# Kernel optimization log

Measured on AMD Instinct MI355X. Metric: run time of the kernel, lower is better.

The kernel has to match this reference:

```python
import jax, jax.numpy as jnp
import numpy as np

D_IN = 2048
H1 = D_IN // 4      # 512
H2 = D_IN // 16     # 128
N_EXP = 8
N_CLS = 10
BATCH = 16384


def setup_inputs() -> dict:
    key = jax.random.key(0)
    ks = jax.random.split(key, 16)
    s = lambda k, shape, fan_in: jax.random.normal(k, shape, jnp.float32) / np.sqrt(fan_in)
    return {
        "fs": jax.random.normal(ks[0], (BATCH, D_IN // 2), jnp.float32),
        "fp": jax.random.normal(ks[1], (BATCH, D_IN // 2), jnp.float32),
        # gate MLP params (output = num_source, softmax)
        "gW1": s(ks[2], (D_IN, H1), D_IN), "gb1": jnp.zeros((H1,), jnp.float32),
        "gW2": s(ks[3], (H1, H2), H1),     "gb2": jnp.zeros((H2,), jnp.float32),
        "gW3": s(ks[4], (H2, N_EXP), H2), "gb3": jnp.zeros((N_EXP,), jnp.float32),
        # stacked expert MLP params (output = num classes, log_softmax)
        "eW1": s(ks[5], (N_EXP, D_IN, H1), D_IN), "eb1": jnp.zeros((N_EXP, H1), jnp.float32),
        "eW2": s(ks[6], (N_EXP, H1, H2), H1),     "eb2": jnp.zeros((N_EXP, H2), jnp.float32),
        "eW3": s(ks[7], (N_EXP, H2, N_CLS), H2),  "eb3": jnp.zeros((N_EXP, N_CLS), jnp.float32),
    }


def reference(fs, fp, gW1, gb1, gW2, gb2, gW3, gb3, eW1, eb1, eW2, eb2, eW3, eb3):
    features = jnp.concatenate([fs, fp], axis=-1)            # [B, D_IN]

    # Gate MLP on detached features (detach is a no-op for fwd), softmax output
    g = jax.nn.relu(features @ gW1 + gb1)
    g = jax.nn.relu(g @ gW2 + gb2)
    gate_outs = jax.nn.softmax(g @ gW3 + gb3, axis=-1)       # [B, E]

    # All experts as batched GEMMs over stacked weights, log_softmax output
    h = jax.nn.relu(jnp.einsum('bd,edh->beh', features, eW1) + eb1[None])   # [B, E, H1]
    h = jax.nn.relu(jnp.einsum('beh,ehk->bek', h, eW2) + eb2[None])         # [B, E, H2]
    logits = jnp.einsum('bek,eko->beo', h, eW3) + eb3[None]                 # [B, E, C]
    expert_outs = jax.nn.log_softmax(logits, axis=-1)                       # [B, E, C]

    # Gate-weighted sum over experts
    output = jnp.einsum('be,bec->bc', gate_outs, expert_outs)               # [B, C]
    return output, gate_outs
```

## Files before the change

kernel.cpp:

```cpp
#include <hip/hip_runtime.h>
#include <hip/hip_bf16.h>

#define B_SZ   16384
#define DIN    2048
#define H1_SZ  512
#define H2_SZ  128
#define N_EXP  8
#define N_CLS  10
#define N1     4608
#define N2     1152

typedef __attribute__((ext_vector_type(8))) __bf16 bf16x8;
typedef __attribute__((ext_vector_type(4))) float  floatx4;
typedef __attribute__((ext_vector_type(4))) short  short4v;
typedef __attribute__((ext_vector_type(8))) short  short8v;

__device__ __forceinline__ float bf2f(short s) {
  unsigned int u = ((unsigned int)(unsigned short)s) << 16;
  float f; __builtin_memcpy(&f, &u, 4); return f;
}

__global__ __launch_bounds__(256) void prep_kernel(
    const float* __restrict__ fs, const float* __restrict__ fp,
    const float* __restrict__ eW1, const float* __restrict__ gW1,
    const float* __restrict__ eW2, const float* __restrict__ gW2,
    __hip_bfloat16* __restrict__ X,
    __hip_bfloat16* __restrict__ W1T,
    __hip_bfloat16* __restrict__ W2T) {
  __shared__ float tbuf[32][33];
  const int b   = blockIdx.x;
  const int tid = threadIdx.x;

  if (b < 2048) {
    const int nf4 = B_SZ * (DIN / 4);
    const float4* fs4 = (const float4*)fs;
    const float4* fp4 = (const float4*)fp;
    for (int i = b * 256 + tid; i < nf4; i += 2048 * 256) {
      int c = i & 511;
      int row = i >> 9;
      float4 v = (c < 256) ? fs4[(size_t)row * 256 + c]
                           : fp4[(size_t)row * 256 + (c - 256)];
      union { short4v v4; __hip_bfloat16 h[4]; } u;
      u.h[0] = __float2bfloat16(v.x);
      u.h[1] = __float2bfloat16(v.y);
      u.h[2] = __float2bfloat16(v.z);
      u.h[3] = __float2bfloat16(v.w);
      *(short4v*)(X + (size_t)i * 4) = u.v4;
    }
  } else {
    const float* esrc; const float* gsrc; __hip_bfloat16* out;
    int K, H, bx, by;
    if (b < 2048 + 9216) {
      int t = b - 2048;  bx = t & 63; by = t >> 6;
      esrc = eW1; gsrc = gW1; out = W1T; K = DIN; H = H1_SZ;
    } else {
      int t = b - 11264; bx = t & 15; by = t >> 4;
      esrc = eW2; gsrc = gW2; out = W2T; K = H1_SZ; H = H2_SZ;
    }
    int k0 = bx * 32, n0 = by * 32;
    int e = n0 / H;
    const float* src; int h0;
    if (e < N_EXP) { src = esrc + (size_t)e * K * H; h0 = n0 - e * H; }
    else           { src = gsrc;                     h0 = n0 - N_EXP * H; }
    int tx = tid & 31, ty = tid >> 5;
    #pragma unroll
    for (int j = 0; j < 4; ++j) {
      int r = ty + j * 8;
      tbuf[r][tx] = src[(size_t)(k0 + r) * H + h0 + tx];
    }
    __syncthreads();
    #pragma unroll
    for (int j = 0; j < 4; ++j) {
      int r = ty + j * 8;
      out[(size_t)(n0 + r) * K + k0 + tx] = __float2bfloat16(tbuf[tx][r]);
    }
  }
}

__device__ __forceinline__ void gemm_core(
    const __hip_bfloat16* __restrict__ A,  int lda,
    const __hip_bfloat16* __restrict__ BT, int K,
    const float* __restrict__ bias,
    __hip_bfloat16* __restrict__ O, int ldo) {
  __shared__ __align__(16) __hip_bfloat16 As[128 * 64];
  __shared__ __align__(16) __hip_bfloat16 Bs[128 * 64];

  const int tid  = threadIdx.x;
  const int lane = tid & 63;
  const int wave = tid >> 6;
  const int wm   = (wave >> 1) * 64;
  const int wn   = (wave & 1) * 64;
  const int lrow  = lane & 15;
  const int lquad = lane >> 4;

  floatx4 acc[4][4] = {};

  for (int k0 = 0; k0 < K; k0 += 64) {
    #pragma unroll
    for (int j = 0; j < 4; ++j) {
      int chunk = j * 256 + tid;
      int mi = chunk >> 3;
      int cs = chunk & 7;
      int cl = cs ^ (mi & 7);
      __builtin_amdgcn_global_load_lds(
          (const __attribute__((address_space(1))) unsigned int*)(A + (size_t)mi * lda + k0 + cl * 8),
          (__attribute__((address_space(3))) unsigned int*)(As + chunk * 8),
          16, 0, 0);
      __builtin_amdgcn_global_load_lds(
          (const __attribute__((address_space(1))) unsigned int*)(BT + (size_t)mi * K + k0 + cl * 8),
          (__attribute__((address_space(3))) unsigned int*)(Bs + chunk * 8),
          16, 0, 0);
    }
    __syncthreads();
    #pragma unroll
    for (int ks = 0; ks < 2; ++ks) {
      bf16x8 a[4], b[4];
      #pragma unroll
      for (int t = 0; t < 4; ++t) {
        int ar = wm + t * 16 + lrow;
        int br = wn + t * 16 + lrow;
        int ca = (ks * 4 + lquad) ^ (ar & 7);
        int cb = (ks * 4 + lquad) ^ (br & 7);
        a[t] = *(const bf16x8*)(As + ar * 64 + ca * 8);
        b[t] = *(const bf16x8*)(Bs + br * 64 + cb * 8);
      }
      #pragma unroll
      for (int mt = 0; mt < 4; ++mt)
        #pragma unroll
        for (int nt = 0; nt < 4; ++nt)
          acc[mt][nt] = __builtin_amdgcn_mfma_f32_16x16x32_bf16(
              a[mt], b[nt], acc[mt][nt], 0, 0, 0);
    }
    __syncthreads();
  }

  #pragma unroll
  for (int nt = 0; nt < 4; ++nt) {
    int col = wn + nt * 16 + lrow;
    float bv = bias[col];
    #pragma unroll
    for (int mt = 0; mt < 4; ++mt) {
      #pragma unroll
      for (int r = 0; r < 4; ++r) {
        int row = wm + mt * 16 + lquad * 4 + r;
        float v = acc[mt][nt][r] + bv;
        v = v > 0.f ? v : 0.f;
        O[(size_t)row * ldo + col] = __float2bfloat16(v);
      }
    }
  }
}

__global__ __launch_bounds__(256, 4) void gemm1_kernel(
    const __hip_bfloat16* __restrict__ X, const __hip_bfloat16* __restrict__ W1T,
    const float* __restrict__ eb1, const float* __restrict__ gb1,
    __hip_bfloat16* __restrict__ H1) {
  int m0 = blockIdx.x * 128;
  int n0 = blockIdx.y * 128;
  const float* bias = (n0 < N_EXP * H1_SZ) ? (eb1 + n0) : (gb1 + (n0 - N_EXP * H1_SZ));
  gemm_core(X + (size_t)m0 * DIN, DIN,
            W1T + (size_t)n0 * DIN, DIN,
            bias,
            H1 + (size_t)m0 * N1 + n0, N1);
}

__global__ __launch_bounds__(256, 4) void gemm2_kernel(
    const __hip_bfloat16* __restrict__ H1, const __hip_bfloat16* __restrict__ W2T,
    const float* __restrict__ eb2, const float* __restrict__ gb2,
    __hip_bfloat16* __restrict__ H2) {
  int m0 = blockIdx.y * 128;
  int z  = blockIdx.z;
  const float* bias = (z < N_EXP) ? (eb2 + z * H2_SZ) : gb2;
  gemm_core(H1 + (size_t)m0 * N1 + z * H1_SZ, N1,
            W2T + (size_t)z * H2_SZ * H1_SZ, H1_SZ,
            bias,
            H2 + (size_t)m0 * N2 + z * H2_SZ, N2);
}

__global__ __launch_bounds__(256) void layer3_kernel(
    const __hip_bfloat16* __restrict__ H2,
    const float* __restrict__ gW3, const float* __restrict__ gb3,
    const float* __restrict__ eW3, const float* __restrict__ eb3,
    float* __restrict__ out, float* __restrict__ gate_out) {
  int tid  = threadIdx.x;
  int j    = tid & 7;
  int rloc = tid >> 3;
  long row = (long)blockIdx.x * 32 + rloc;
  const __hip_bfloat16* hrow = H2 + row * N2;

  float accg = 0.f;
  float acc[N_CLS];
  #pragma unroll
  for (int c = 0; c < N_CLS; ++c) acc[c] = 0.f;

  #pragma unroll 4
  for (int k8 = 0; k8 < 16; ++k8) {
    short8v hg8 = *(const short8v*)(hrow + N_EXP * H2_SZ + k8 * 8);
    short8v he8 = *(const short8v*)(hrow + j * H2_SZ + k8 * 8);
    #pragma unroll
    for (int t = 0; t < 8; ++t) {
      int k = k8 * 8 + t;
      float hg = bf2f(hg8[t]);
      float he = bf2f(he8[t]);
      accg += hg * gW3[k * N_EXP + j];
      const float* w = eW3 + (size_t)(j * H2_SZ + k) * N_CLS;
      #pragma unroll
      for (int c = 0; c < N_CLS; ++c) acc[c] += he * w[c];
    }
  }

  float gj = accg + gb3[j];
  float mx = gj;
  mx = fmaxf(mx, __shfl_xor(mx, 1));
  mx = fmaxf(mx, __shfl_xor(mx, 2));
  mx = fmaxf(mx, __shfl_xor(mx, 4));
  float ex = __expf(gj - mx);
  float s = ex;
  s += __shfl_xor(s, 1);
  s += __shfl_xor(s, 2);
  s += __shfl_xor(s, 4);
  float gp = ex / s;

  float lg[N_CLS];
  float lm = -1e30f;
  #pragma unroll
  for (int c = 0; c < N_CLS; ++c) {
    lg[c] = acc[c] + eb3[j * N_CLS + c];
    lm = fmaxf(lm, lg[c]);
  }
  float es = 0.f;
  #pragma unroll
  for (int c = 0; c < N_CLS; ++c) es += __expf(lg[c] - lm);
  float lse = lm + __logf(es);

  float o[N_CLS];
  #pragma unroll
  for (int c = 0; c < N_CLS; ++c) o[c] = gp * (lg[c] - lse);
  #pragma unroll
  for (int c = 0; c < N_CLS; ++c) {
    o[c] += __shfl_xor(o[c], 1);
    o[c] += __shfl_xor(o[c], 2);
    o[c] += __shfl_xor(o[c], 4);
  }

  gate_out[row * N_EXP + j] = gp;
  if (j == 0) {
    #pragma unroll
    for (int c = 0; c < N_CLS; ++c) out[row * N_CLS + c] = o[c];
  }
}

extern "C" void kernel_launch(void* const* d_in, const int* in_sizes, int n_in,
                              void* d_out, int out_size, void* d_ws, size_t ws_size,
                              hipStream_t stream) {
  const float* fs  = (const float*)d_in[0];
  const float* fp  = (const float*)d_in[1];
  const float* gW1 = (const float*)d_in[2];
  const float* gb1 = (const float*)d_in[3];
  const float* gW2 = (const float*)d_in[4];
  const float* gb2 = (const float*)d_in[5];
  const float* gW3 = (const float*)d_in[6];
  const float* gb3 = (const float*)d_in[7];
  const float* eW1 = (const float*)d_in[8];
  const float* eb1 = (const float*)d_in[9];
  const float* eW2 = (const float*)d_in[10];
  const float* eb2 = (const float*)d_in[11];
  const float* eW3 = (const float*)d_in[12];
  const float* eb3 = (const float*)d_in[13];
  float* out = (float*)d_out;

  char* ws = (char*)d_ws;
  __hip_bfloat16* X   = (__hip_bfloat16*)ws;
  __hip_bfloat16* H2  = X;
  __hip_bfloat16* W1T = (__hip_bfloat16*)(ws + 67108864);
  __hip_bfloat16* W2T = (__hip_bfloat16*)(ws + 85983232);
  __hip_bfloat16* H1  = (__hip_bfloat16*)(ws + 87162880);

  prep_kernel<<<11840, 256, 0, stream>>>(fs, fp, eW1, gW1, eW2, gW2, X, W1T, W2T);
  gemm1_kernel<<<dim3(B_SZ / 128, N1 / 128), 256, 0, stream>>>(X, W1T, eb1, gb1, H1);
  gemm2_kernel<<<dim3(1, B_SZ / 128, N_EXP + 1), 256, 0, stream>>>(H1, W2T, eb2, gb2, H2);
  layer3_kernel<<<B_SZ / 32, 256, 0, stream>>>(H2, gW3, gb3, eW3, eb3,
                                               out, out + (size_t)B_SZ * N_CLS);
}
```

Baseline: 612.2 us.

## Fuse all stages into one persistent kernel with grid barriers and atomic tile scheduling

Replaces the four launches (prep, gemm1, gemm2, layer3) with one persistent kernel of 1024 blocks. The stages are separated by software grid barriers built on atomic counters, and GEMM tiles are handed out dynamically through an atomic counter. The aim is to remove launch gaps and tail effects between kernels. The counters live in the gate_out region, which is zeroed by a memset and later overwritten by the final stage. It risks deadlock if the 1024 blocks cannot all be resident at once, and the barrier spinning adds overhead. The tile order also changes from m-fastest to n-fastest, which alters L2 reuse.

```diff
diff --git a/kernel.cpp b/kernel.cpp
--- a/kernel.cpp
+++ b/kernel.cpp
@@ -9,6 +9,7 @@
 #define N_CLS  10
 #define N1     4608
 #define N2     1152
+#define NBLK   1024
 
 typedef __attribute__((ext_vector_type(8))) __bf16 bf16x8;
 typedef __attribute__((ext_vector_type(4))) float  floatx4;
@@ -20,71 +21,30 @@
   float f; __builtin_memcpy(&f, &u, 4); return f;
 }
 
-__global__ __launch_bounds__(256) void prep_kernel(
-    const float* __restrict__ fs, const float* __restrict__ fp,
-    const float* __restrict__ eW1, const float* __restrict__ gW1,
-    const float* __restrict__ eW2, const float* __restrict__ gW2,
-    __hip_bfloat16* __restrict__ X,
-    __hip_bfloat16* __restrict__ W1T,
-    __hip_bfloat16* __restrict__ W2T) {
-  __shared__ float tbuf[32][33];
-  const int b   = blockIdx.x;
-  const int tid = threadIdx.x;
-
-  if (b < 2048) {
-    const int nf4 = B_SZ * (DIN / 4);
-    const float4* fs4 = (const float4*)fs;
-    const float4* fp4 = (const float4*)fp;
-    for (int i = b * 256 + tid; i < nf4; i += 2048 * 256) {
-      int c = i & 511;
-      int row = i >> 9;
-      float4 v = (c < 256) ? fs4[(size_t)row * 256 + c]
-                           : fp4[(size_t)row * 256 + (c - 256)];
-      union { short4v v4; __hip_bfloat16 h[4]; } u;
-      u.h[0] = __float2bfloat16(v.x);
-      u.h[1] = __float2bfloat16(v.y);
-      u.h[2] = __float2bfloat16(v.z);
-      u.h[3] = __float2bfloat16(v.w);
-      *(short4v*)(X + (size_t)i * 4) = u.v4;
-    }
-  } else {
-    const float* esrc; const float* gsrc; __hip_bfloat16* out;
-    int K, H, bx, by;
-    if (b < 2048 + 9216) {
-      int t = b - 2048;  bx = t & 63; by = t >> 6;
-      esrc = eW1; gsrc = gW1; out = W1T; K = DIN; H = H1_SZ;
+__device__ __forceinline__ void grid_barrier(unsigned* cnt, unsigned* flag) {
+  __syncthreads();
+  if (threadIdx.x == 0) {
+    __threadfence();
+    unsigned prev = __hip_atomic_fetch_add(cnt, 1u, __ATOMIC_ACQ_REL,
+                                           __HIP_MEMORY_SCOPE_AGENT);
+    if (prev == NBLK - 1) {
+      __hip_atomic_store(flag, 1u, __ATOMIC_RELEASE, __HIP_MEMORY_SCOPE_AGENT);
     } else {
-      int t = b - 11264; bx = t & 15; by = t >> 4;
-      esrc = eW2; gsrc = gW2; out = W2T; K = H1_SZ; H = H2_SZ;
-    }
-    int k0 = bx * 32, n0 = by * 32;
-    int e = n0 / H;
-    const float* src; int h0;
-    if (e < N_EXP) { src = esrc + (size_t)e * K * H; h0 = n0 - e * H; }
-    else           { src = gsrc;                     h0 = n0 - N_EXP * H; }
-    int tx = tid & 31, ty = tid >> 5;
-    #pragma unroll
-    for (int j = 0; j < 4; ++j) {
-      int r = ty + j * 8;
-      tbuf[r][tx] = src[(size_t)(k0 + r) * H + h0 + tx];
-    }
-    __syncthreads();
-    #pragma unroll
-    for (int j = 0; j < 4; ++j) {
-      int r = ty + j * 8;
-      out[(size_t)(n0 + r) * K + k0 + tx] = __float2bfloat16(tbuf[tx][r]);
-    }
-  }
-}
-
-__device__ __forceinline__ void gemm_core(
-    const __hip_bfloat16* __restrict__ A,  int lda,
-    const __hip_bfloat16* __restrict__ BT, int K,
-    const float* __restrict__ bias,
-    __hip_bfloat16* __restrict__ O, int ldo) {
-  __shared__ __align__(16) __hip_bfloat16 As[128 * 64];
-  __shared__ __align__(16) __hip_bfloat16 Bs[128 * 64];
-
+      while (__hip_atomic_load(flag, __ATOMIC_ACQUIRE,
+                               __HIP_MEMORY_SCOPE_AGENT) == 0u)
+        __builtin_amdgcn_s_sleep(2);
+    }
+    __threadfence();
+  }
+  __syncthreads();
+}
+
+__device__ __forceinline__ void gemm_tile(
+    const __hip_bfloat16* A,  int lda,
+    const __hip_bfloat16* BT, int K,
+    const float* bias,
+    __hip_bfloat16* O, int ldo,
+    __hip_bfloat16* As, __hip_bfloat16* Bs) {
   const int tid  = threadIdx.x;
   const int lane = tid & 63;
   const int wave = tid >> 6;
@@ -151,102 +111,179 @@
   }
 }
 
-__global__ __launch_bounds__(256, 4) void gemm1_kernel(
-    const __hip_bfloat16* __restrict__ X, const __hip_bfloat16* __restrict__ W1T,
-    const float* __restrict__ eb1, const float* __restrict__ gb1,
-    __hip_bfloat16* __restrict__ H1) {
-  int m0 = blockIdx.x * 128;
-  int n0 = blockIdx.y * 128;
-  const float* bias = (n0 < N_EXP * H1_SZ) ? (eb1 + n0) : (gb1 + (n0 - N_EXP * H1_SZ));
-  gemm_core(X + (size_t)m0 * DIN, DIN,
-            W1T + (size_t)n0 * DIN, DIN,
-            bias,
-            H1 + (size_t)m0 * N1 + n0, N1);
-}
-
-__global__ __launch_bounds__(256, 4) void gemm2_kernel(
-    const __hip_bfloat16* __restrict__ H1, const __hip_bfloat16* __restrict__ W2T,
-    const float* __restrict__ eb2, const float* __restrict__ gb2,
-    __hip_bfloat16* __restrict__ H2) {
-  int m0 = blockIdx.y * 128;
-  int z  = blockIdx.z;
-  const float* bias = (z < N_EXP) ? (eb2 + z * H2_SZ) : gb2;
-  gemm_core(H1 + (size_t)m0 * N1 + z * H1_SZ, N1,
-            W2T + (size_t)z * H2_SZ * H1_SZ, H1_SZ,
-            bias,
-            H2 + (size_t)m0 * N2 + z * H2_SZ, N2);
-}
-
-__global__ __launch_bounds__(256) void layer3_kernel(
-    const __hip_bfloat16* __restrict__ H2,
+__global__ __launch_bounds__(256, 4) void mega_kernel(
+    const float* __restrict__ fs, const float* __restrict__ fp,
+    const float* __restrict__ gW1, const float* __restrict__ gb1,
+    const float* __restrict__ gW2, const float* __restrict__ gb2,
     const float* __restrict__ gW3, const float* __restrict__ gb3,
+    const float* __restrict__ eW1, const float* __restrict__ eb1,
+    const float* __restrict__ eW2, const float* __restrict__ eb2,
     const float* __restrict__ eW3, const float* __restrict__ eb3,
-    float* __restrict__ out, float* __restrict__ gate_out) {
-  int tid  = threadIdx.x;
-  int j    = tid & 7;
-  int rloc = tid >> 3;
-  long row = (long)blockIdx.x * 32 + rloc;
-  const __hip_bfloat16* hrow = H2 + row * N2;
-
-  float accg = 0.f;
-  float acc[N_CLS];
-  #pragma unroll
-  for (int c = 0; c < N_CLS; ++c) acc[c] = 0.f;
-
-  #pragma unroll 4
-  for (int k8 = 0; k8 < 16; ++k8) {
-    short8v hg8 = *(const short8v*)(hrow + N_EXP * H2_SZ + k8 * 8);
-    short8v he8 = *(const short8v*)(hrow + j * H2_SZ + k8 * 8);
-    #pragma unroll
-    for (int t = 0; t < 8; ++t) {
-      int k = k8 * 8 + t;
-      float hg = bf2f(hg8[t]);
-      float he = bf2f(he8[t]);
-      accg += hg * gW3[k * N_EXP + j];
-      const float* w = eW3 + (size_t)(j * H2_SZ + k) * N_CLS;
-      #pragma unroll
-      for (int c = 0; c < N_CLS; ++c) acc[c] += he * w[c];
-    }
-  }
-
-  float gj = accg + gb3[j];
-  float mx = gj;
-  mx = fmaxf(mx, __shfl_xor(mx, 1));
-  mx = fmaxf(mx, __shfl_xor(mx, 2));
-  mx = fmaxf(mx, __shfl_xor(mx, 4));
-  float ex = __expf(gj - mx);
-  float s = ex;
-  s += __shfl_xor(s, 1);
-  s += __shfl_xor(s, 2);
-  s += __shfl_xor(s, 4);
-  float gp = ex / s;
-
-  float lg[N_CLS];
-  float lm = -1e30f;
-  #pragma unroll
-  for (int c = 0; c < N_CLS; ++c) {
-    lg[c] = acc[c] + eb3[j * N_CLS + c];
-    lm = fmaxf(lm, lg[c]);
-  }
-  float es = 0.f;
-  #pragma unroll
-  for (int c = 0; c < N_CLS; ++c) es += __expf(lg[c] - lm);
-  float lse = lm + __logf(es);
-
-  float o[N_CLS];
-  #pragma unroll
-  for (int c = 0; c < N_CLS; ++c) o[c] = gp * (lg[c] - lse);
-  #pragma unroll
-  for (int c = 0; c < N_CLS; ++c) {
-    o[c] += __shfl_xor(o[c], 1);
-    o[c] += __shfl_xor(o[c], 2);
-    o[c] += __shfl_xor(o[c], 4);
-  }
-
-  gate_out[row * N_EXP + j] = gp;
-  if (j == 0) {
-    #pragma unroll
-    for (int c = 0; c < N_CLS; ++c) out[row * N_CLS + c] = o[c];
+    __hip_bfloat16* X,
+    __hip_bfloat16* W1T, __hip_bfloat16* W2T,
+    __hip_bfloat16* H1,  __hip_bfloat16* H2,
+    float* out, float* gate_out, unsigned* ctr) {
+  __shared__ __align__(16) __hip_bfloat16 smem[2 * 128 * 64];
+  __hip_bfloat16* As = smem;
+  __hip_bfloat16* Bs = smem + 128 * 64;
+  __shared__ int s_t;
+
+  const int pid = blockIdx.x;
+  const int tid = threadIdx.x;
+
+  {
+    const int nf4 = B_SZ * (DIN / 4);
+    const float4* fs4 = (const float4*)fs;
+    const float4* fp4 = (const float4*)fp;
+    for (int i = pid * 256 + tid; i < nf4; i += NBLK * 256) {
+      int c = i & 511;
+      int row = i >> 9;
+      float4 v = (c < 256) ? fs4[(size_t)row * 256 + c]
+                           : fp4[(size_t)row * 256 + (c - 256)];
+      union { short4v v4; __hip_bfloat16 h[4]; } u;
+      u.h[0] = __float2bfloat16(v.x);
+      u.h[1] = __float2bfloat16(v.y);
+      u.h[2] = __float2bfloat16(v.z);
+      u.h[3] = __float2bfloat16(v.w);
+      *(short4v*)(X + (size_t)i * 4) = u.v4;
+    }
+  }
+  {
+    float (*tbuf)[33] = (float(*)[33])smem;
+    const int NT1 = 64 * 144;
+    const int NT2 = 16 * 36;
+    int tx = tid & 31, ty = tid >> 5;
+    for (int t = pid; t < NT1 + NT2; t += NBLK) {
+      const float* esrc; const float* gsrc; __hip_bfloat16* o;
+      int K, H, bx, by;
+      if (t < NT1) { bx = t & 63; by = t >> 6; esrc = eW1; gsrc = gW1; o = W1T; K = DIN;   H = H1_SZ; }
+      else { int q = t - NT1; bx = q & 15; by = q >> 4; esrc = eW2; gsrc = gW2; o = W2T; K = H1_SZ; H = H2_SZ; }
+      int k0 = bx * 32, n0 = by * 32;
+      int e = n0 / H;
+      const float* src; int h0;
+      if (e < N_EXP) { src = esrc + (size_t)e * K * H; h0 = n0 - e * H; }
+      else           { src = gsrc;                     h0 = n0 - N_EXP * H; }
+      __syncthreads();
+      #pragma unroll
+      for (int j = 0; j < 4; ++j) {
+        int r = ty + j * 8;
+        tbuf[r][tx] = src[(size_t)(k0 + r) * H + h0 + tx];
+      }
+      __syncthreads();
+      #pragma unroll
+      for (int j = 0; j < 4; ++j) {
+        int r = ty + j * 8;
+        o[(size_t)(n0 + r) * K + k0 + tx] = __float2bfloat16(tbuf[tx][r]);
+      }
+    }
+  }
+
+  grid_barrier(ctr + 0, ctr + 1);
+
+  for (;;) {
+    __syncthreads();
+    if (tid == 0)
+      s_t = (int)__hip_atomic_fetch_add(&ctr[6], 1u, __ATOMIC_RELAXED,
+                                        __HIP_MEMORY_SCOPE_AGENT);
+    __syncthreads();
+    int t = s_t;
+    if (t >= 36 * 128) break;
+    int nt = t % 36, mt = t / 36;
+    int n0 = nt * 128, m0 = mt * 128;
+    const float* bias = (n0 < N_EXP * H1_SZ) ? (eb1 + n0) : (gb1 + (n0 - N_EXP * H1_SZ));
+    gemm_tile(X + (size_t)m0 * DIN, DIN,
+              W1T + (size_t)n0 * DIN, DIN,
+              bias,
+              H1 + (size_t)m0 * N1 + n0, N1, As, Bs);
+  }
+
+  grid_barrier(ctr + 2, ctr + 3);
+
+  for (;;) {
+    __syncthreads();
+    if (tid == 0)
+      s_t = (int)__hip_atomic_fetch_add(&ctr[7], 1u, __ATOMIC_RELAXED,
+                                        __HIP_MEMORY_SCOPE_AGENT);
+    __syncthreads();
+    int t = s_t;
+    if (t >= 128 * (N_EXP + 1)) break;
+    int mt = t & 127, z = t >> 7;
+    int m0 = mt * 128;
+    const float* bias = (z < N_EXP) ? (eb2 + z * H2_SZ) : gb2;
+    gemm_tile(H1 + (size_t)m0 * N1 + z * H1_SZ, N1,
+              W2T + (size_t)z * H2_SZ * H1_SZ, H1_SZ,
+              bias,
+              H2 + (size_t)m0 * N2 + z * H2_SZ, N2, As, Bs);
+  }
+
+  grid_barrier(ctr + 4, ctr + 5);
+
+  for (int g = pid; g < B_SZ / 32; g += NBLK) {
+    int j    = tid & 7;
+    int rloc = tid >> 3;
+    long row = (long)g * 32 + rloc;
+    const __hip_bfloat16* hrow = H2 + row * N2;
+
+    float accg = 0.f;
+    float acc[N_CLS];
+    #pragma unroll
+    for (int c = 0; c < N_CLS; ++c) acc[c] = 0.f;
+
+    #pragma unroll 4
+    for (int k8 = 0; k8 < 16; ++k8) {
+      short8v hg8 = *(const short8v*)(hrow + N_EXP * H2_SZ + k8 * 8);
+      short8v he8 = *(const short8v*)(hrow + j * H2_SZ + k8 * 8);
+      #pragma unroll
+      for (int t = 0; t < 8; ++t) {
+        int k = k8 * 8 + t;
+        float hg = bf2f(hg8[t]);
+        float he = bf2f(he8[t]);
+        accg += hg * gW3[k * N_EXP + j];
+        const float* w = eW3 + (size_t)(j * H2_SZ + k) * N_CLS;
+        #pragma unroll
+        for (int c = 0; c < N_CLS; ++c) acc[c] += he * w[c];
+      }
+    }
+
+    float gj = accg + gb3[j];
+    float mx = gj;
+    mx = fmaxf(mx, __shfl_xor(mx, 1));
+    mx = fmaxf(mx, __shfl_xor(mx, 2));
+    mx = fmaxf(mx, __shfl_xor(mx, 4));
+    float ex = __expf(gj - mx);
+    float s = ex;
+    s += __shfl_xor(s, 1);
+    s += __shfl_xor(s, 2);
+    s += __shfl_xor(s, 4);
+    float gp = ex / s;
+
+    float lg[N_CLS];
+    float lm = -1e30f;
+    #pragma unroll
+    for (int c = 0; c < N_CLS; ++c) {
+      lg[c] = acc[c] + eb3[j * N_CLS + c];
+      lm = fmaxf(lm, lg[c]);
+    }
+    float es = 0.f;
+    #pragma unroll
+    for (int c = 0; c < N_CLS; ++c) es += __expf(lg[c] - lm);
+    float lse = lm + __logf(es);
+
+    float o[N_CLS];
+    #pragma unroll
+    for (int c = 0; c < N_CLS; ++c) o[c] = gp * (lg[c] - lse);
+    #pragma unroll
+    for (int c = 0; c < N_CLS; ++c) {
+      o[c] += __shfl_xor(o[c], 1);
+      o[c] += __shfl_xor(o[c], 2);
+      o[c] += __shfl_xor(o[c], 4);
+    }
+
+    gate_out[row * N_EXP + j] = gp;
+    if (j == 0) {
+      #pragma unroll
+      for (int c = 0; c < N_CLS; ++c) out[row * N_CLS + c] = o[c];
+    }
   }
 }
 
@@ -268,6 +305,7 @@
   const float* eW3 = (const float*)d_in[12];
   const float* eb3 = (const float*)d_in[13];
   float* out = (float*)d_out;
+  float* gate_out = out + (size_t)B_SZ * N_CLS;
 
   char* ws = (char*)d_ws;
   __hip_bfloat16* X   = (__hip_bfloat16*)ws;
@@ -276,9 +314,11 @@
   __hip_bfloat16* W2T = (__hip_bfloat16*)(ws + 85983232);
   __hip_bfloat16* H1  = (__hip_bfloat16*)(ws + 87162880);
 
-  prep_kernel<<<11840, 256, 0, stream>>>(fs, fp, eW1, gW1, eW2, gW2, X, W1T, W2T);
-  gemm1_kernel<<<dim3(B_SZ / 128, N1 / 128), 256, 0, stream>>>(X, W1T, eb1, gb1, H1);
-  gemm2_kernel<<<dim3(1, B_SZ / 128, N_EXP + 1), 256, 0, stream>>>(H1, W2T, eb2, gb2, H2);
-  layer3_kernel<<<B_SZ / 32, 256, 0, stream>>>(H2, gW3, gb3, eW3, eb3,
-                                               out, out + (size_t)B_SZ * N_CLS);
-}
+  unsigned* ctr = (unsigned*)gate_out;
+  hipMemsetAsync(ctr, 0, 64, stream);
+
+  mega_kernel<<<NBLK, 256, 0, stream>>>(
+      fs, fp, gW1, gb1, gW2, gb2, gW3, gb3,
+      eW1, eb1, eW2, eb2, eW3, eb3,
+      X, W1T, W2T, H1, H2, out, gate_out, ctr);
+}
```

Measured after the change: 2.052 ms. 235% more time.

## Fuse layer-2 GEMM with layer-3 heads and swap gemm1 grid order

Applied to the files above, without the earlier changes.

Replaces the separate gemm2 and layer3 kernels with one kernel that, for each block of 64 rows, loops over the 9 expert/gate slices. Each slice's layer-2 output stays in LDS and is immediately reduced to logits, so the H2 round trip through global memory and one launch are removed. gemm1 is inlined and its grid is transposed so consecutive blocks share the same row tile of X. In exchange the fused kernel has only 256 blocks with large LDS use, and its layer-3 step is scalar FMA over LDS, which risks low occupancy and serial latency.

```diff
diff --git a/kernel.cpp b/kernel.cpp
--- a/kernel.cpp
+++ b/kernel.cpp
@@ -77,11 +77,10 @@
   }
 }
 
-__device__ __forceinline__ void gemm_core(
-    const __hip_bfloat16* __restrict__ A,  int lda,
-    const __hip_bfloat16* __restrict__ BT, int K,
-    const float* __restrict__ bias,
-    __hip_bfloat16* __restrict__ O, int ldo) {
+__global__ __launch_bounds__(256, 4) void gemm1_kernel(
+    const __hip_bfloat16* __restrict__ X, const __hip_bfloat16* __restrict__ W1T,
+    const float* __restrict__ eb1, const float* __restrict__ gb1,
+    __hip_bfloat16* __restrict__ H1) {
   __shared__ __align__(16) __hip_bfloat16 As[128 * 64];
   __shared__ __align__(16) __hip_bfloat16 Bs[128 * 64];
 
@@ -93,9 +92,16 @@
   const int lrow  = lane & 15;
   const int lquad = lane >> 4;
 
+  const int m0 = blockIdx.y * 128;
+  const int n0 = blockIdx.x * 128;
+  const float* bias = (n0 < N_EXP * H1_SZ) ? (eb1 + n0) : (gb1 + (n0 - N_EXP * H1_SZ));
+  const __hip_bfloat16* A  = X   + (size_t)m0 * DIN;
+  const __hip_bfloat16* BT = W1T + (size_t)n0 * DIN;
+  __hip_bfloat16* O = H1 + (size_t)m0 * N1 + n0;
+
   floatx4 acc[4][4] = {};
 
-  for (int k0 = 0; k0 < K; k0 += 64) {
+  for (int k0 = 0; k0 < DIN; k0 += 64) {
     #pragma unroll
     for (int j = 0; j < 4; ++j) {
       int chunk = j * 256 + tid;
@@ -103,11 +109,11 @@
       int cs = chunk & 7;
       int cl = cs ^ (mi & 7);
       __builtin_amdgcn_global_load_lds(
-          (const __attribute__((address_space(1))) unsigned int*)(A + (size_t)mi * lda + k0 + cl * 8),
+          (const __attribute__((address_space(1))) unsigned int*)(A + (size_t)mi * DIN + k0 + cl * 8),
           (__attribute__((address_space(3))) unsigned int*)(As + chunk * 8),
           16, 0, 0);
       __builtin_amdgcn_global_load_lds(
-          (const __attribute__((address_space(1))) unsigned int*)(BT + (size_t)mi * K + k0 + cl * 8),
+          (const __attribute__((address_space(1))) unsigned int*)(BT + (size_t)mi * DIN + k0 + cl * 8),
           (__attribute__((address_space(3))) unsigned int*)(Bs + chunk * 8),
           16, 0, 0);
     }
@@ -145,108 +151,168 @@
         int row = wm + mt * 16 + lquad * 4 + r;
         float v = acc[mt][nt][r] + bv;
         v = v > 0.f ? v : 0.f;
-        O[(size_t)row * ldo + col] = __float2bfloat16(v);
-      }
-    }
-  }
-}
-
-__global__ __launch_bounds__(256, 4) void gemm1_kernel(
-    const __hip_bfloat16* __restrict__ X, const __hip_bfloat16* __restrict__ W1T,
-    const float* __restrict__ eb1, const float* __restrict__ gb1,
-    __hip_bfloat16* __restrict__ H1) {
-  int m0 = blockIdx.x * 128;
-  int n0 = blockIdx.y * 128;
-  const float* bias = (n0 < N_EXP * H1_SZ) ? (eb1 + n0) : (gb1 + (n0 - N_EXP * H1_SZ));
-  gemm_core(X + (size_t)m0 * DIN, DIN,
-            W1T + (size_t)n0 * DIN, DIN,
-            bias,
-            H1 + (size_t)m0 * N1 + n0, N1);
-}
-
-__global__ __launch_bounds__(256, 4) void gemm2_kernel(
+        O[(size_t)row * N1 + col] = __float2bfloat16(v);
+      }
+    }
+  }
+}
+
+__global__ __launch_bounds__(256, 2) void fused23_kernel(
     const __hip_bfloat16* __restrict__ H1, const __hip_bfloat16* __restrict__ W2T,
     const float* __restrict__ eb2, const float* __restrict__ gb2,
-    __hip_bfloat16* __restrict__ H2) {
-  int m0 = blockIdx.y * 128;
-  int z  = blockIdx.z;
-  const float* bias = (z < N_EXP) ? (eb2 + z * H2_SZ) : gb2;
-  gemm_core(H1 + (size_t)m0 * N1 + z * H1_SZ, N1,
-            W2T + (size_t)z * H2_SZ * H1_SZ, H1_SZ,
-            bias,
-            H2 + (size_t)m0 * N2 + z * H2_SZ, N2);
-}
-
-__global__ __launch_bounds__(256) void layer3_kernel(
-    const __hip_bfloat16* __restrict__ H2,
     const float* __restrict__ gW3, const float* __restrict__ gb3,
     const float* __restrict__ eW3, const float* __restrict__ eb3,
     float* __restrict__ out, float* __restrict__ gate_out) {
-  int tid  = threadIdx.x;
-  int j    = tid & 7;
-  int rloc = tid >> 3;
-  long row = (long)blockIdx.x * 32 + rloc;
-  const __hip_bfloat16* hrow = H2 + row * N2;
-
-  float accg = 0.f;
-  float acc[N_CLS];
-  #pragma unroll
-  for (int c = 0; c < N_CLS; ++c) acc[c] = 0.f;
-
-  #pragma unroll 4
-  for (int k8 = 0; k8 < 16; ++k8) {
-    short8v hg8 = *(const short8v*)(hrow + N_EXP * H2_SZ + k8 * 8);
-    short8v he8 = *(const short8v*)(hrow + j * H2_SZ + k8 * 8);
-    #pragma unroll
-    for (int t = 0; t < 8; ++t) {
-      int k = k8 * 8 + t;
-      float hg = bf2f(hg8[t]);
-      float he = bf2f(he8[t]);
-      accg += hg * gW3[k * N_EXP + j];
-      const float* w = eW3 + (size_t)(j * H2_SZ + k) * N_CLS;
-      #pragma unroll
-      for (int c = 0; c < N_CLS; ++c) acc[c] += he * w[c];
-    }
-  }
-
-  float gj = accg + gb3[j];
-  float mx = gj;
-  mx = fmaxf(mx, __shfl_xor(mx, 1));
-  mx = fmaxf(mx, __shfl_xor(mx, 2));
-  mx = fmaxf(mx, __shfl_xor(mx, 4));
-  float ex = __expf(gj - mx);
-  float s = ex;
-  s += __shfl_xor(s, 1);
-  s += __shfl_xor(s, 2);
-  s += __shfl_xor(s, 4);
-  float gp = ex / s;
-
-  float lg[N_CLS];
-  float lm = -1e30f;
-  #pragma unroll
-  for (int c = 0; c < N_CLS; ++c) {
-    lg[c] = acc[c] + eb3[j * N_CLS + c];
-    lm = fmaxf(lm, lg[c]);
-  }
-  float es = 0.f;
-  #pragma unroll
-  for (int c = 0; c < N_CLS; ++c) es += __expf(lg[c] - lm);
-  float lse = lm + __logf(es);
-
-  float o[N_CLS];
-  #pragma unroll
-  for (int c = 0; c < N_CLS; ++c) o[c] = gp * (lg[c] - lse);
-  #pragma unroll
-  for (int c = 0; c < N_CLS; ++c) {
-    o[c] += __shfl_xor(o[c], 1);
-    o[c] += __shfl_xor(o[c], 2);
-    o[c] += __shfl_xor(o[c], 4);
-  }
-
-  gate_out[row * N_EXP + j] = gp;
-  if (j == 0) {
-    #pragma unroll
-    for (int c = 0; c < N_CLS; ++c) out[row * N_CLS + c] = o[c];
+  __shared__ __align__(16) __hip_bfloat16 As[64 * 64];
+  __shared__ __align__(16) __hip_bfloat16 Bs[128 * 64];
+  __shared__ __align__(16) __hip_bfloat16 H2L[64 * 130];
+  __shared__ float logitsL[64][90];
+
+  const int tid  = threadIdx.x;
+  const int lane = tid & 63;
+  const int wave = tid >> 6;
+  const int wm2  = (wave >> 1) * 32;
+  const int wn2  = (wave & 1) * 64;
+  const int lrow  = lane & 15;
+  const int lquad = lane >> 4;
+  const int m0 = blockIdx.x * 64;
+
+  const int grow = tid >> 2;
+  const int gpart = tid & 3;
+
+  for (int z = 0; z < N_EXP + 1; ++z) {
+    const __hip_bfloat16* A  = H1  + (size_t)m0 * N1 + z * H1_SZ;
+    const __hip_bfloat16* BT = W2T + (size_t)z * H2_SZ * H1_SZ;
+    const float* bias2 = (z < N_EXP) ? (eb2 + z * H2_SZ) : gb2;
+
+    floatx4 acc[2][4] = {};
+    for (int k0 = 0; k0 < H1_SZ; k0 += 64) {
+      #pragma unroll
+      for (int j = 0; j < 2; ++j) {
+        int chunk = j * 256 + tid;
+        int mi = chunk >> 3, cs = chunk & 7, cl = cs ^ (mi & 7);
+        __builtin_amdgcn_global_load_lds(
+            (const __attribute__((address_space(1))) unsigned int*)(A + (size_t)mi * N1 + k0 + cl * 8),
+            (__attribute__((address_space(3))) unsigned int*)(As + chunk * 8),
+            16, 0, 0);
+      }
+      #pragma unroll
+      for (int j = 0; j < 4; ++j) {
+        int idx = j * 256 + tid;
+        int row = idx >> 3, cs = idx & 7, cl = cs ^ (row & 7);
+        __builtin_amdgcn_global_load_lds(
+            (const __attribute__((address_space(1))) unsigned int*)(BT + (size_t)row * H1_SZ + k0 + cl * 8),
+            (__attribute__((address_space(3))) unsigned int*)(Bs + idx * 8),
+            16, 0, 0);
+      }
+      __syncthreads();
+      #pragma unroll
+      for (int ks = 0; ks < 2; ++ks) {
+        bf16x8 a[2], b[4];
+        #pragma unroll
+        for (int t = 0; t < 2; ++t) {
+          int ar = wm2 + t * 16 + lrow;
+          int ca = (ks * 4 + lquad) ^ (ar & 7);
+          a[t] = *(const bf16x8*)(As + ar * 64 + ca * 8);
+        }
+        #pragma unroll
+        for (int t = 0; t < 4; ++t) {
+          int br = wn2 + t * 16 + lrow;
+          int cb = (ks * 4 + lquad) ^ (br & 7);
+          b[t] = *(const bf16x8*)(Bs + br * 64 + cb * 8);
+        }
+        #pragma unroll
+        for (int mt = 0; mt < 2; ++mt)
+          #pragma unroll
+          for (int nt = 0; nt < 4; ++nt)
+            acc[mt][nt] = __builtin_amdgcn_mfma_f32_16x16x32_bf16(
+                a[mt], b[nt], acc[mt][nt], 0, 0, 0);
+      }
+      __syncthreads();
+    }
+
+    #pragma unroll
+    for (int nt = 0; nt < 4; ++nt) {
+      int col = wn2 + nt * 16 + lrow;
+      float bv = bias2[col];
+      #pragma unroll
+      for (int mt = 0; mt < 2; ++mt) {
+        #pragma unroll
+        for (int r = 0; r < 4; ++r) {
+          int row = wm2 + mt * 16 + lquad * 4 + r;
+          float v = acc[mt][nt][r] + bv;
+          v = v > 0.f ? v : 0.f;
+          H2L[row * 130 + col] = __float2bfloat16(v);
+        }
+      }
+    }
+    __syncthreads();
+
+    if (z < N_EXP) {
+      float accv[3] = {0.f, 0.f, 0.f};
+      const float* w = eW3 + (size_t)z * H2_SZ * N_CLS;
+      for (int k = 0; k < H2_SZ; ++k) {
+        float h = bf2f(*(const short*)(H2L + grow * 130 + k));
+        #pragma unroll
+        for (int i = 0; i < 3; ++i) {
+          int c = gpart + 4 * i;
+          if (c < N_CLS) accv[i] += h * w[k * N_CLS + c];
+        }
+      }
+      #pragma unroll
+      for (int i = 0; i < 3; ++i) {
+        int c = gpart + 4 * i;
+        if (c < N_CLS)
+          logitsL[grow][8 + z * 10 + c] = accv[i] + eb3[z * N_CLS + c];
+      }
+    } else {
+      float accv[2] = {0.f, 0.f};
+      for (int k = 0; k < H2_SZ; ++k) {
+        float h = bf2f(*(const short*)(H2L + grow * 130 + k));
+        #pragma unroll
+        for (int i = 0; i < 2; ++i)
+          accv[i] += h * gW3[k * N_EXP + gpart + 4 * i];
+      }
+      #pragma unroll
+      for (int i = 0; i < 2; ++i)
+        logitsL[grow][gpart + 4 * i] = accv[i] + gb3[gpart + 4 * i];
+    }
+  }
+  __syncthreads();
+
+  if (tid < 64) {
+    const float* L = logitsL[tid];
+    long row = m0 + tid;
+    float mx = L[0];
+    #pragma unroll
+    for (int j = 1; j < 8; ++j) mx = fmaxf(mx, L[j]);
+    float gs = 0.f, gp[8];
+    #pragma unroll
+    for (int j = 0; j < 8; ++j) { gp[j] = __expf(L[j] - mx); gs += gp[j]; }
+    float inv = 1.f / gs;
+    #pragma unroll
+    for (int j = 0; j < 8; ++j) gp[j] *= inv;
+
+    float ov[N_CLS];
+    #pragma unroll
+    for (int c = 0; c < N_CLS; ++c) ov[c] = 0.f;
+    #pragma unroll
+    for (int j = 0; j < 8; ++j) {
+      const float* lg = L + 8 + j * 10;
+      float lm = lg[0];
+      #pragma unroll
+      for (int c = 1; c < N_CLS; ++c) lm = fmaxf(lm, lg[c]);
+      float es = 0.f;
+      #pragma unroll
+      for (int c = 0; c < N_CLS; ++c) es += __expf(lg[c] - lm);
+      float lse = lm + __logf(es);
+      #pragma unroll
+      for (int c = 0; c < N_CLS; ++c) ov[c] += gp[j] * (lg[c] - lse);
+    }
+    #pragma unroll
+    for (int c = 0; c < N_CLS; ++c) out[row * N_CLS + c] = ov[c];
+    #pragma unroll
+    for (int j = 0; j < 8; ++j) gate_out[row * N_EXP + j] = gp[j];
   }
 }
 
@@ -268,17 +334,17 @@
   const float* eW3 = (const float*)d_in[12];
   const float* eb3 = (const float*)d_in[13];
   float* out = (float*)d_out;
+  float* gate_out = out + (size_t)B_SZ * N_CLS;
 
   char* ws = (char*)d_ws;
   __hip_bfloat16* X   = (__hip_bfloat16*)ws;
-  __hip_bfloat16* H2  = X;
   __hip_bfloat16* W1T = (__hip_bfloat16*)(ws + 67108864);
   __hip_bfloat16* W2T = (__hip_bfloat16*)(ws + 85983232);
   __hip_bfloat16* H1  = (__hip_bfloat16*)(ws + 87162880);
 
   prep_kernel<<<11840, 256, 0, stream>>>(fs, fp, eW1, gW1, eW2, gW2, X, W1T, W2T);
-  gemm1_kernel<<<dim3(B_SZ / 128, N1 / 128), 256, 0, stream>>>(X, W1T, eb1, gb1, H1);
-  gemm2_kernel<<<dim3(1, B_SZ / 128, N_EXP + 1), 256, 0, stream>>>(H1, W2T, eb2, gb2, H2);
-  layer3_kernel<<<B_SZ / 32, 256, 0, stream>>>(H2, gW3, gb3, eW3, eb3,
-                                               out, out + (size_t)B_SZ * N_CLS);
-}
+  gemm1_kernel<<<dim3(N1 / 128, B_SZ / 128), 256, 0, stream>>>(X, W1T, eb1, gb1, H1);
+  fused23_kernel<<<B_SZ / 64, 256, 0, stream>>>(H1, W2T, eb2, gb2,
+                                                gW3, gb3, eW3, eb3,
+                                                out, gate_out);
+}
```

Result: slower. 743.8 us (+21.5%).
